# Optimization experiments

Hardware: AMD Instinct MI355X
Metric: run time of the kernel (lower is better)

The kernel has to match this reference:

```python
import jax, jax.numpy as jnp
import numpy as np

NINP, NHID, NPROJ, NLAYER = 240, 1024, 512, 3


def setup_inputs() -> dict:
    key = jax.random.key(0)
    keys = jax.random.split(key, 1 + NLAYER * 6)
    inp = {"x": jax.random.normal(keys[0], (500, 32, NINP), dtype=jnp.float32)}
    kit = iter(keys[1:])
    for l in range(NLAYER):
        nin = NINP if l == 0 else NPROJ
        s = 1.0 / np.sqrt(nin + NPROJ)
        inp[f"W{l}"] = jax.random.uniform(next(kit), (4 * NHID, nin + NPROJ), minval=-s, maxval=s, dtype=jnp.float32)
        inp[f"b{l}"] = jax.random.uniform(next(kit), (4 * NHID,), minval=-s, maxval=s, dtype=jnp.float32)
        sp = 1.0 / np.sqrt(NHID)
        inp[f"P{l}"] = jax.random.uniform(next(kit), (NPROJ, NHID), minval=-sp, maxval=sp, dtype=jnp.float32)
        inp[f"pi{l}"] = jax.random.normal(next(kit), (NHID,), dtype=jnp.float32) * 0.1
        inp[f"pf{l}"] = jax.random.normal(next(kit), (NHID,), dtype=jnp.float32) * 0.1
        inp[f"po{l}"] = jax.random.normal(next(kit), (NHID,), dtype=jnp.float32) * 0.1
    return inp


def _lstmp_layer(x, W, b, P, pi, pf, po):
    # x: [T, B, nin]; returns [T, B, nproj]
    T, B, _ = x.shape
    h0 = jnp.zeros((B, NPROJ), x.dtype)
    c0 = jnp.zeros((B, NHID), x.dtype)

    def step(carry, xt):
        hx, cx = carry
        gates = jnp.concatenate([xt, hx], axis=1) @ W.T + b  # [B, 4*nhid]
        c_in, i_g, f_g, o_g = jnp.split(gates, 4, axis=1)
        i_g = jax.nn.sigmoid(i_g + pi * cx)
        f_g = jax.nn.sigmoid(f_g + pf * cx)
        cy = jnp.clip(f_g * cx + i_g * jnp.tanh(c_in), -50.0, 50.0)
        o_g = jax.nn.sigmoid(o_g + po * cy)
        hy = (o_g * jnp.tanh(cy)) @ P.T  # [B, nproj]
        return (hy, cy), hy

    _, ys = jax.lax.scan(step, (h0, c0), x)
    return ys


def reference(x, W0, b0, P0, pi0, pf0, po0, W1, b1, P1, pi1, pf1, po1, W2, b2, P2, pi2, pf2, po2):
    y = _lstmp_layer(x, W0, b0, P0, pi0, pf0, po0)
    y = _lstmp_layer(y, W1, b1, P1, pi1, pf1, po1)
    y = _lstmp_layer(y, W2, b2, P2, pi2, pf2, po2)
    return y
```

## Files before the change

kernel.cpp:

```cpp
#include <hip/hip_runtime.h>


typedef short s16x4 __attribute__((ext_vector_type(4)));
typedef short s16x8 __attribute__((ext_vector_type(8)));
typedef float f32x4 __attribute__((ext_vector_type(4)));

#define MFMA16(a,b,c) __builtin_amdgcn_mfma_f32_16x16x32_bf16((a),(b),(c),0,0,0)

__device__ __forceinline__ unsigned short f2bf(float f) {
  unsigned int u = __builtin_bit_cast(unsigned int, f);
  u += 0x7FFFu + ((u >> 16) & 1u);
  return (unsigned short)(u >> 16);
}
__device__ __forceinline__ float bf2f(unsigned short h) {
  unsigned int u = ((unsigned int)h) << 16;
  return __builtin_bit_cast(float, u);
}
__device__ __forceinline__ float fsig(float x)  { return __fdividef(1.0f, 1.0f + __expf(-x)); }
__device__ __forceinline__ float ftanh(float x) { return 1.0f - __fdividef(2.0f, 1.0f + __expf(2.0f * x)); }

__device__ __forceinline__ void bload16(s16x8* dst, const unsigned short* p) {
  asm volatile("global_load_dwordx4 %0, %1, off sc1"
               : "=v"(*dst) : "v"(p) : "memory");
}
__device__ __forceinline__ void bwait() {
  asm volatile("s_waitcnt vmcnt(0)" ::: "memory");
  __builtin_amdgcn_sched_barrier(0);
}
__device__ __forceinline__ void bstore16(unsigned short* p, s16x8 v) {
  asm volatile("global_store_dwordx4 %0, %1, off sc1"
               :: "v"(p), "v"(v) : "memory");
}

__device__ __forceinline__ unsigned int cnt_load(const unsigned int* p) {
  return __hip_atomic_load(p, __ATOMIC_RELAXED, __HIP_MEMORY_SCOPE_AGENT);
}
__device__ __forceinline__ void cnt_add(unsigned int* p) {
  __hip_atomic_fetch_add(p, 1u, __ATOMIC_RELAXED, __HIP_MEMORY_SCOPE_AGENT);
}

__device__ __forceinline__ void gbar(unsigned int* bar, unsigned int* rel, unsigned int seq) {
  __syncthreads();
  asm volatile("" ::: "memory");
  if (blockIdx.x == 0) {
    const int tid = threadIdx.x;
    if (tid > 0 && tid < 192) {
      while (__hip_atomic_load(&bar[tid * 16], __ATOMIC_RELAXED, __HIP_MEMORY_SCOPE_AGENT) != seq) {
        __builtin_amdgcn_s_sleep(1);
      }
    }
    __syncthreads();
    if (tid == 0) {
      __hip_atomic_store(rel, seq, __ATOMIC_RELAXED, __HIP_MEMORY_SCOPE_AGENT);
    }
  } else {
    if (threadIdx.x == 0) {
      __hip_atomic_store(&bar[blockIdx.x * 16], seq, __ATOMIC_RELAXED, __HIP_MEMORY_SCOPE_AGENT);
      while (__hip_atomic_load(rel, __ATOMIC_RELAXED, __HIP_MEMORY_SCOPE_AGENT) != seq) {
        __builtin_amdgcn_s_sleep(1);
      }
    }
    __syncthreads();
  }
  asm volatile("" ::: "memory");
}

__global__ __launch_bounds__(512, 2) void lstmp_persist(
    const float* __restrict__ x,
    const float* __restrict__ W0, const float* __restrict__ b0, const float* __restrict__ P0,
    const float* __restrict__ pi0, const float* __restrict__ pf0, const float* __restrict__ po0,
    const float* __restrict__ W1, const float* __restrict__ b1, const float* __restrict__ P1,
    const float* __restrict__ pi1, const float* __restrict__ pf1, const float* __restrict__ po1,
    const float* __restrict__ W2, const float* __restrict__ b2, const float* __restrict__ P2,
    const float* __restrict__ pi2, const float* __restrict__ pf2, const float* __restrict__ po2,
    float* __restrict__ out, unsigned char* __restrict__ ws)
{
  const int tid  = threadIdx.x;
  const int bid  = blockIdx.x;
  const int lane = tid & 63;
  const int wv   = tid >> 6;
  const int quad8 = (lane >> 4) * 8;
  const int nrow  = lane & 15;

  unsigned int* bar   = (unsigned int*)ws;
  unsigned int* rel   = bar + 4096;
  unsigned int* gcnt  = rel + 32;
  unsigned int* mcnt  = gcnt + 128;
  unsigned short* xhi = (unsigned short*)(ws + 20480);
  unsigned short* xlo  = xhi  + 4096000;
  unsigned short* hhi  = xlo  + 4096000;
  unsigned short* hlo  = hhi  + 98304;
  unsigned short* mhi  = hlo  + 98304;
  unsigned short* mlo  = mhi  + 98304;

  const float* Wsrc[3] = {W0, W1, W2};
  const float* Psrc[3] = {P0, P1, P2};
  const float* Bsrc[3] = {b0, b1, b2};
  const float* PIs[3]  = {pi0, pi1, pi2};
  const float* PFs[3]  = {pf0, pf1, pf2};
  const float* POs[3]  = {po0, po1, po2};

  __shared__ float exch[8][4][512];
  __shared__ float c_lds[512];
  __shared__ float lds_pad[4096];
  ((volatile float*)lds_pad)[tid & 4095] = 0.0f;
  unsigned short* mst = (unsigned short*)lds_pad;
  unsigned short* hst = mst + 1024;

  const unsigned int NT = 192u * 512u;
  const unsigned int gtid = (unsigned int)bid * 512u + (unsigned int)tid;

  const int lA  = bid >> 6;
  const int utA = bid & 63;
  const int ptC = (bid & 63) >> 1;
  const int mtC = bid & 1;

  const int nkbinA  = (lA == 0) ? 8   : 16;
  const int kinpadA = (lA == 0) ? 256 : 512;
  const int kbwA    = (lA == 0) ? 3   : 4;
  const int kwA     = (lA == 0) ? 752 : 1024;
  const int ninA    = (lA == 0) ? 240 : 512;
  const int kb0     = wv * kbwA;

  for (unsigned int i = gtid; i < 4096000u; i += NT) {
    unsigned int k = i & 255u, tb = i >> 8;
    float v = (k < 240u) ? x[tb * 240u + k] : 0.0f;
    unsigned short h = f2bf(v);
    xhi[i] = h; xlo[i] = f2bf(v - bf2f(h));
  }
  for (unsigned int i = gtid; i < 98304u; i += NT) { hhi[i] = 0; hlo[i] = 0; }
  for (unsigned int i = gtid; i < 640u; i += NT) gcnt[i] = 0u;
  c_lds[tid] = 0.0f;

  s16x8 wgh[4][4], wgl[4][4];
  {
    const float* Wl = Wsrc[lA];
    #pragma unroll
    for (int j = 0; j < 4; ++j) {
      if (j < kbwA) {
        const int kbase = (kb0 + j) * 32 + quad8;
        #pragma unroll
        for (int g = 0; g < 4; ++g) {
          const size_t r = (size_t)((g * 64 + utA) * 16 + nrow);
          #pragma unroll
          for (int jj = 0; jj < 8; ++jj) {
            const int k = kbase + jj;
            float v;
            if (k < kinpadA) v = (lA == 0 && k >= 240) ? 0.0f : Wl[r * kwA + k];
            else             v = Wl[r * kwA + (k - kinpadA + ninA)];
            unsigned short h = f2bf(v);
            wgh[j][g][jj] = (short)h;
            wgl[j][g][jj] = (short)f2bf(v - bf2f(h));
          }
        }
      } else {
        #pragma unroll
        for (int g = 0; g < 4; ++g) { wgh[j][g] = (s16x8)0; wgl[j][g] = (s16x8)0; }
      }
    }
  }
  s16x8 wph[4], wpl[4];
  {
    const float* Pl = Psrc[lA];
    const size_t prow = (size_t)(ptC * 16 + nrow);
    #pragma unroll
    for (int j = 0; j < 4; ++j) {
      const int kbase = (wv * 4 + j) * 32 + quad8;
      #pragma unroll
      for (int jj = 0; jj < 8; ++jj) {
        float v = Pl[prow * 1024u + (size_t)(kbase + jj)];
        unsigned short h = f2bf(v);
        wph[j][jj] = (short)h;
        wpl[j][jj] = (short)f2bf(v - bf2f(h));
      }
    }
  }
  const int uc = utA * 16 + (tid & 15);
  const float rbc = Bsrc[lA][uc];
  const float rbi = Bsrc[lA][1024 + uc];
  const float rbf = Bsrc[lA][2048 + uc];
  const float rbo = Bsrc[lA][3072 + uc];
  const float rpi = PIs[lA][uc];
  const float rpf = PFs[lA][uc];
  const float rpo = POs[lA][uc];

  __builtin_amdgcn_fence(__ATOMIC_RELEASE, "agent");
  gbar(bar, rel, 1u);
  __builtin_amdgcn_fence(__ATOMIC_ACQUIRE, "agent");

  for (int s = 0; s < 502; ++s) {
    const int t = s - lA;
    const bool act = (t >= 0) && (t < 500);
    const int rbuf = (s + 1) & 1;
    const int wbuf = s & 1;

    if (act) {
      const unsigned short* hbh = hhi + rbuf * 49152;
      const unsigned short* hbl = hlo + rbuf * 49152;

      s16x8 fh0[4], fl0[4], fh1[4], fl1[4];
      #pragma unroll
      for (int j = 0; j < 4; ++j) {
        if (j < kbwA) {
          const int kb = kb0 + j;
          if (kb < nkbinA) {
            if (lA == 0) {
              const unsigned short* ph = xhi + (size_t)(t * 32 + nrow) * 256 + kb * 32 + quad8;
              const unsigned short* pl = xlo + (size_t)(t * 32 + nrow) * 256 + kb * 32 + quad8;
              fh0[j] = *(const s16x8*)ph; fh1[j] = *(const s16x8*)(ph + 16 * 256);
              fl0[j] = *(const s16x8*)pl; fl1[j] = *(const s16x8*)(pl + 16 * 256);
            } else {
              const unsigned short* ph = hbh + (size_t)((lA - 1) * 32 + nrow) * 512 + kb * 32 + quad8;
              const unsigned short* pl = hbl + (size_t)((lA - 1) * 32 + nrow) * 512 + kb * 32 + quad8;
              bload16(&fh0[j], ph); bload16(&fh1[j], ph + 16 * 512);
              bload16(&fl0[j], pl); bload16(&fl1[j], pl + 16 * 512);
            }
          } else {
            const int ko = kb * 32 + quad8 - kinpadA;
            const unsigned short* ph = hbh + (size_t)(lA * 32 + nrow) * 512 + ko;
            const unsigned short* pl = hbl + (size_t)(lA * 32 + nrow) * 512 + ko;
            bload16(&fh0[j], ph); bload16(&fh1[j], ph + 16 * 512);
            bload16(&fl0[j], pl); bload16(&fl1[j], pl + 16 * 512);
          }
        }
      }
      bwait();

      f32x4 acc[4][2];
      #pragma unroll
      for (int g = 0; g < 4; ++g) { acc[g][0] = {0.f,0.f,0.f,0.f}; acc[g][1] = {0.f,0.f,0.f,0.f}; }

      #pragma unroll
      for (int j = 0; j < 4; ++j) {
        if (j < kbwA) {
          #pragma unroll
          for (int g = 0; g < 4; ++g) {
            acc[g][0] = MFMA16(fh0[j], wgh[j][g], acc[g][0]);
            acc[g][0] = MFMA16(fl0[j], wgh[j][g], acc[g][0]);
            acc[g][0] = MFMA16(fh0[j], wgl[j][g], acc[g][0]);
            acc[g][1] = MFMA16(fh1[j], wgh[j][g], acc[g][1]);
            acc[g][1] = MFMA16(fl1[j], wgh[j][g], acc[g][1]);
            acc[g][1] = MFMA16(fh1[j], wgl[j][g], acc[g][1]);
          }
        }
      }
      #pragma unroll
      for (int g = 0; g < 4; ++g) {
        #pragma unroll
        for (int r = 0; r < 4; ++r) {
          const int m0 = (lane >> 4) * 4 + r;
          exch[wv][g][m0 * 16 + (lane & 15)]        = acc[g][0][r];
          exch[wv][g][(m0 + 16) * 16 + (lane & 15)] = acc[g][1][r];
        }
      }
      __syncthreads();

      {
        const int e = tid;
        float sc = 0.f, si = 0.f, sf = 0.f, so = 0.f;
        #pragma unroll
        for (int w = 0; w < 8; ++w) {
          sc += exch[w][0][e]; si += exch[w][1][e];
          sf += exch[w][2][e]; so += exch[w][3][e];
        }
        const float cin = sc + rbc;
        const float gi  = si + rbi;
        const float gf  = sf + rbf;
        const float go  = so + rbo;
        const float cx  = c_lds[e];
        const float ig  = fsig(gi + rpi * cx);
        const float fg  = fsig(gf + rpf * cx);
        float cy = fg * cx + ig * ftanh(cin);
        cy = fminf(50.0f, fmaxf(-50.0f, cy));
        const float og = fsig(go + rpo * cy);
        const float mv = og * ftanh(cy);
        c_lds[e] = cy;
        const unsigned short mh = f2bf(mv);
        mst[e]       = mh;
        mst[512 + e] = f2bf(mv - bf2f(mh));
      }
      __syncthreads();
      if (tid < 128) {
        const int plane = tid >> 6;
        const int r2 = tid & 63;
        const int bl = r2 >> 1, half = r2 & 1;
        s16x8 v = *(const s16x8*)(mst + plane * 512 + bl * 16 + half * 8);
        unsigned short* dst = (plane ? mlo : mhi) + (size_t)(lA * 32 + bl) * 1024 + utA * 16 + half * 8;
        bstore16(dst, v);
        asm volatile("s_waitcnt vmcnt(0)" ::: "memory");
      }
      __syncthreads();
      if (tid == 0) cnt_add(&mcnt[lA * 128 + (utA & 3) * 32]);

      if (tid == 0) {
        const unsigned int want = 64u * (unsigned int)(t + 1);
        const unsigned int* mp = mcnt + lA * 128;
        for (;;) {
          unsigned int sum = cnt_load(mp) + cnt_load(mp + 32) + cnt_load(mp + 64) + cnt_load(mp + 96);
          if (sum >= want) break;
          __builtin_amdgcn_s_sleep(1);
        }
      }
      __syncthreads();

      const unsigned short* mah = mhi + (size_t)(lA * 32 + mtC * 16 + nrow) * 1024;
      const unsigned short* mal = mlo + (size_t)(lA * 32 + mtC * 16 + nrow) * 1024;

      s16x8 fmh[4], fml[4];
      #pragma unroll
      for (int j = 0; j < 4; ++j) {
        const int ko = (wv * 4 + j) * 32 + quad8;
        bload16(&fmh[j], mah + ko);
        bload16(&fml[j], mal + ko);
      }
      bwait();

      f32x4 pacc = {0.f, 0.f, 0.f, 0.f};
      #pragma unroll
      for (int j = 0; j < 4; ++j) {
        pacc = MFMA16(fmh[j], wph[j], pacc);
        pacc = MFMA16(fml[j], wph[j], pacc);
        pacc = MFMA16(fmh[j], wpl[j], pacc);
      }
      #pragma unroll
      for (int r = 0; r < 4; ++r) {
        exch[wv][0][((lane >> 4) * 4 + r) * 16 + (lane & 15)] = pacc[r];
      }
      __syncthreads();
      if (tid < 256) {
        float v = 0.f;
        #pragma unroll
        for (int w = 0; w < 8; ++w) v += exch[w][0][tid];
        const unsigned short hh = f2bf(v);
        hst[tid]       = hh;
        hst[256 + tid] = f2bf(v - bf2f(hh));
        if (lA == 2) {
          const int b = mtC * 16 + (tid >> 4);
          const int p = ptC * 16 + (tid & 15);
          out[((size_t)t * 32 + b) * 512 + p] = v;
        }
      }
      __syncthreads();
      if (tid < 64) {
        const int plane = tid >> 5;
        const int r2 = tid & 31;
        const int bl = r2 >> 1, half = r2 & 1;
        s16x8 v = *(const s16x8*)(hst + plane * 256 + bl * 16 + half * 8);
        unsigned short* dst = (plane ? hlo : hhi) + (size_t)wbuf * 49152
                            + (size_t)(lA * 32 + mtC * 16 + bl) * 512 + ptC * 16 + half * 8;
        bstore16(dst, v);
        asm volatile("s_waitcnt vmcnt(0)" ::: "memory");
      }
    }
    __syncthreads();
    if (tid == 0) {
      cnt_add(&gcnt[(bid & 3) * 32]);
      const unsigned int want = 192u * (unsigned int)(s + 1);
      for (;;) {
        unsigned int sum = cnt_load(gcnt) + cnt_load(gcnt + 32) + cnt_load(gcnt + 64) + cnt_load(gcnt + 96);
        if (sum >= want) break;
        __builtin_amdgcn_s_sleep(1);
      }
    }
    __syncthreads();
  }
}

extern "C" void kernel_launch(void* const* d_in, const int* in_sizes, int n_in,
                              void* d_out, int out_size, void* d_ws, size_t ws_size,
                              hipStream_t stream) {
  const float* x   = (const float*)d_in[0];
  const float* W0  = (const float*)d_in[1];
  const float* b0  = (const float*)d_in[2];
  const float* P0  = (const float*)d_in[3];
  const float* pi0 = (const float*)d_in[4];
  const float* pf0 = (const float*)d_in[5];
  const float* po0 = (const float*)d_in[6];
  const float* W1  = (const float*)d_in[7];
  const float* b1  = (const float*)d_in[8];
  const float* P1  = (const float*)d_in[9];
  const float* pi1 = (const float*)d_in[10];
  const float* pf1 = (const float*)d_in[11];
  const float* po1 = (const float*)d_in[12];
  const float* W2  = (const float*)d_in[13];
  const float* b2  = (const float*)d_in[14];
  const float* P2  = (const float*)d_in[15];
  const float* pi2 = (const float*)d_in[16];
  const float* pf2 = (const float*)d_in[17];
  const float* po2 = (const float*)d_in[18];

  hipLaunchKernelGGL(lstmp_persist, dim3(192), dim3(512), 0, stream,
                     x, W0, b0, P0, pi0, pf0, po0,
                     W1, b1, P1, pi1, pf1, po1,
                     W2, b2, P2, pi2, pf2, po2,
                     (float*)d_out, (unsigned char*)d_ws);
}
```

Before: 8.106 ms.

## Replace global per-step barrier with per-layer counters and 4-deep h buffers

Removes the grid-wide barrier that every block joined at each wavefront step. Each layer group now waits only on its own layer's previous step, the upstream layer's current output, and the downstream layer's progress (back-pressure). Hidden state buffers grow from 2 to 4 slots so layers can drift apart by several timesteps without overwriting data still being read. This decouples the three layers' pipelines and lowers synchronization stalls, at the cost of more workspace and more complex ordering logic.

After: 8.025 ms. Within noise of the previous version (-1.0%).

```diff
diff --git a/kernel.cpp b/kernel.cpp
--- a/kernel.cpp
+++ b/kernel.cpp
@@ -37,6 +37,13 @@
 }
 __device__ __forceinline__ void cnt_add(unsigned int* p) {
   __hip_atomic_fetch_add(p, 1u, __ATOMIC_RELAXED, __HIP_MEMORY_SCOPE_AGENT);
+}
+__device__ __forceinline__ void poll4(const unsigned int* p, unsigned int want) {
+  for (;;) {
+    unsigned int s = cnt_load(p) + cnt_load(p + 32) + cnt_load(p + 64) + cnt_load(p + 96);
+    if (s >= want) break;
+    __builtin_amdgcn_s_sleep(1);
+  }
 }
 
 __device__ __forceinline__ void gbar(unsigned int* bar, unsigned int* rel, unsigned int seq) {
@@ -84,13 +91,13 @@
 
   unsigned int* bar   = (unsigned int*)ws;
   unsigned int* rel   = bar + 4096;
-  unsigned int* gcnt  = rel + 32;
-  unsigned int* mcnt  = gcnt + 128;
+  unsigned int* lcnt  = rel + 32;
+  unsigned int* mcnt  = lcnt + 384;
   unsigned short* xhi = (unsigned short*)(ws + 20480);
   unsigned short* xlo  = xhi  + 4096000;
   unsigned short* hhi  = xlo  + 4096000;
-  unsigned short* hlo  = hhi  + 98304;
-  unsigned short* mhi  = hlo  + 98304;
+  unsigned short* hlo  = hhi  + 196608;
+  unsigned short* mhi  = hlo  + 196608;
   unsigned short* mlo  = mhi  + 98304;
 
   const float* Wsrc[3] = {W0, W1, W2};
@@ -128,8 +135,8 @@
     unsigned short h = f2bf(v);
     xhi[i] = h; xlo[i] = f2bf(v - bf2f(h));
   }
-  for (unsigned int i = gtid; i < 98304u; i += NT) { hhi[i] = 0; hlo[i] = 0; }
-  for (unsigned int i = gtid; i < 640u; i += NT) gcnt[i] = 0u;
+  for (unsigned int i = gtid; i < 196608u; i += NT) { hhi[i] = 0; hlo[i] = 0; }
+  for (unsigned int i = gtid; i < 768u; i += NT) lcnt[i] = 0u;
   c_lds[tid] = 0.0f;
 
   s16x8 wgh[4][4], wgl[4][4];
@@ -188,181 +195,173 @@
   gbar(bar, rel, 1u);
   __builtin_amdgcn_fence(__ATOMIC_ACQUIRE, "agent");
 
-  for (int s = 0; s < 502; ++s) {
-    const int t = s - lA;
-    const bool act = (t >= 0) && (t < 500);
-    const int rbuf = (s + 1) & 1;
-    const int wbuf = s & 1;
-
-    if (act) {
-      const unsigned short* hbh = hhi + rbuf * 49152;
-      const unsigned short* hbl = hlo + rbuf * 49152;
-
-      s16x8 fh0[4], fl0[4], fh1[4], fl1[4];
-      #pragma unroll
-      for (int j = 0; j < 4; ++j) {
-        if (j < kbwA) {
-          const int kb = kb0 + j;
-          if (kb < nkbinA) {
-            if (lA == 0) {
-              const unsigned short* ph = xhi + (size_t)(t * 32 + nrow) * 256 + kb * 32 + quad8;
-              const unsigned short* pl = xlo + (size_t)(t * 32 + nrow) * 256 + kb * 32 + quad8;
-              fh0[j] = *(const s16x8*)ph; fh1[j] = *(const s16x8*)(ph + 16 * 256);
-              fl0[j] = *(const s16x8*)pl; fl1[j] = *(const s16x8*)(pl + 16 * 256);
-            } else {
-              const unsigned short* ph = hbh + (size_t)((lA - 1) * 32 + nrow) * 512 + kb * 32 + quad8;
-              const unsigned short* pl = hbl + (size_t)((lA - 1) * 32 + nrow) * 512 + kb * 32 + quad8;
-              bload16(&fh0[j], ph); bload16(&fh1[j], ph + 16 * 512);
-              bload16(&fl0[j], pl); bload16(&fl1[j], pl + 16 * 512);
-            }
+  for (int t = 0; t < 500; ++t) {
+    if (tid == 0) {
+      poll4(lcnt + lA * 128, 64u * (unsigned int)t);
+      if (lA > 0) poll4(lcnt + (lA - 1) * 128, 64u * (unsigned int)(t + 1));
+      if (lA < 2 && t >= 4) poll4(lcnt + (lA + 1) * 128, 64u * (unsigned int)(t - 3));
+    }
+    __syncthreads();
+
+    const unsigned short* hRecH = hhi + (size_t)(((t + 3) & 3) * 49152 + lA * 16384);
+    const unsigned short* hRecL = hlo + (size_t)(((t + 3) & 3) * 49152 + lA * 16384);
+    const unsigned short* hInH  = hhi + (size_t)((t & 3) * 49152 + (lA - 1) * 16384);
+    const unsigned short* hInL  = hlo + (size_t)((t & 3) * 49152 + (lA - 1) * 16384);
+
+    s16x8 fh0[4], fl0[4], fh1[4], fl1[4];
+    #pragma unroll
+    for (int j = 0; j < 4; ++j) {
+      if (j < kbwA) {
+        const int kb = kb0 + j;
+        if (kb < nkbinA) {
+          if (lA == 0) {
+            const unsigned short* ph = xhi + (size_t)(t * 32 + nrow) * 256 + kb * 32 + quad8;
+            const unsigned short* pl = xlo + (size_t)(t * 32 + nrow) * 256 + kb * 32 + quad8;
+            fh0[j] = *(const s16x8*)ph; fh1[j] = *(const s16x8*)(ph + 16 * 256);
+            fl0[j] = *(const s16x8*)pl; fl1[j] = *(const s16x8*)(pl + 16 * 256);
           } else {
-            const int ko = kb * 32 + quad8 - kinpadA;
-            const unsigned short* ph = hbh + (size_t)(lA * 32 + nrow) * 512 + ko;
-            const unsigned short* pl = hbl + (size_t)(lA * 32 + nrow) * 512 + ko;
+            const unsigned short* ph = hInH + (size_t)nrow * 512 + kb * 32 + quad8;
+            const unsigned short* pl = hInL + (size_t)nrow * 512 + kb * 32 + quad8;
             bload16(&fh0[j], ph); bload16(&fh1[j], ph + 16 * 512);
             bload16(&fl0[j], pl); bload16(&fl1[j], pl + 16 * 512);
           }
+        } else {
+          const int ko = kb * 32 + quad8 - kinpadA;
+          const unsigned short* ph = hRecH + (size_t)nrow * 512 + ko;
+          const unsigned short* pl = hRecL + (size_t)nrow * 512 + ko;
+          bload16(&fh0[j], ph); bload16(&fh1[j], ph + 16 * 512);
+          bload16(&fl0[j], pl); bload16(&fl1[j], pl + 16 * 512);
         }
       }
-      bwait();
-
-      f32x4 acc[4][2];
-      #pragma unroll
-      for (int g = 0; g < 4; ++g) { acc[g][0] = {0.f,0.f,0.f,0.f}; acc[g][1] = {0.f,0.f,0.f,0.f}; }
-
-      #pragma unroll
-      for (int j = 0; j < 4; ++j) {
-        if (j < kbwA) {
-          #pragma unroll
-          for (int g = 0; g < 4; ++g) {
-            acc[g][0] = MFMA16(fh0[j], wgh[j][g], acc[g][0]);
-            acc[g][0] = MFMA16(fl0[j], wgh[j][g], acc[g][0]);
-            acc[g][0] = MFMA16(fh0[j], wgl[j][g], acc[g][0]);
-            acc[g][1] = MFMA16(fh1[j], wgh[j][g], acc[g][1]);
-            acc[g][1] = MFMA16(fl1[j], wgh[j][g], acc[g][1]);
-            acc[g][1] = MFMA16(fh1[j], wgl[j][g], acc[g][1]);
-          }
+    }
+    bwait();
+
+    f32x4 acc[4][2];
+    #pragma unroll
+    for (int g = 0; g < 4; ++g) { acc[g][0] = {0.f,0.f,0.f,0.f}; acc[g][1] = {0.f,0.f,0.f,0.f}; }
+
+    #pragma unroll
+    for (int j = 0; j < 4; ++j) {
+      if (j < kbwA) {
+        #pragma unroll
+        for (int g = 0; g < 4; ++g) {
+          acc[g][0] = MFMA16(fh0[j], wgh[j][g], acc[g][0]);
+          acc[g][0] = MFMA16(fl0[j], wgh[j][g], acc[g][0]);
+          acc[g][0] = MFMA16(fh0[j], wgl[j][g], acc[g][0]);
+          acc[g][1] = MFMA16(fh1[j], wgh[j][g], acc[g][1]);
+          acc[g][1] = MFMA16(fl1[j], wgh[j][g], acc[g][1]);
+          acc[g][1] = MFMA16(fh1[j], wgl[j][g], acc[g][1]);
         }
       }
-      #pragma unroll
-      for (int g = 0; g < 4; ++g) {
-        #pragma unroll
-        for (int r = 0; r < 4; ++r) {
-          const int m0 = (lane >> 4) * 4 + r;
-          exch[wv][g][m0 * 16 + (lane & 15)]        = acc[g][0][r];
-          exch[wv][g][(m0 + 16) * 16 + (lane & 15)] = acc[g][1][r];
-        }
-      }
-      __syncthreads();
-
-      {
-        const int e = tid;
-        float sc = 0.f, si = 0.f, sf = 0.f, so = 0.f;
-        #pragma unroll
-        for (int w = 0; w < 8; ++w) {
-          sc += exch[w][0][e]; si += exch[w][1][e];
-          sf += exch[w][2][e]; so += exch[w][3][e];
-        }
-        const float cin = sc + rbc;
-        const float gi  = si + rbi;
-        const float gf  = sf + rbf;
-        const float go  = so + rbo;
-        const float cx  = c_lds[e];
-        const float ig  = fsig(gi + rpi * cx);
-        const float fg  = fsig(gf + rpf * cx);
-        float cy = fg * cx + ig * ftanh(cin);
-        cy = fminf(50.0f, fmaxf(-50.0f, cy));
-        const float og = fsig(go + rpo * cy);
-        const float mv = og * ftanh(cy);
-        c_lds[e] = cy;
-        const unsigned short mh = f2bf(mv);
-        mst[e]       = mh;
-        mst[512 + e] = f2bf(mv - bf2f(mh));
-      }
-      __syncthreads();
-      if (tid < 128) {
-        const int plane = tid >> 6;
-        const int r2 = tid & 63;
-        const int bl = r2 >> 1, half = r2 & 1;
-        s16x8 v = *(const s16x8*)(mst + plane * 512 + bl * 16 + half * 8);
-        unsigned short* dst = (plane ? mlo : mhi) + (size_t)(lA * 32 + bl) * 1024 + utA * 16 + half * 8;
-        bstore16(dst, v);
-        asm volatile("s_waitcnt vmcnt(0)" ::: "memory");
-      }
-      __syncthreads();
-      if (tid == 0) cnt_add(&mcnt[lA * 128 + (utA & 3) * 32]);
-
-      if (tid == 0) {
-        const unsigned int want = 64u * (unsigned int)(t + 1);
-        const unsigned int* mp = mcnt + lA * 128;
-        for (;;) {
-          unsigned int sum = cnt_load(mp) + cnt_load(mp + 32) + cnt_load(mp + 64) + cnt_load(mp + 96);
-          if (sum >= want) break;
-          __builtin_amdgcn_s_sleep(1);
-        }
-      }
-      __syncthreads();
-
-      const unsigned short* mah = mhi + (size_t)(lA * 32 + mtC * 16 + nrow) * 1024;
-      const unsigned short* mal = mlo + (size_t)(lA * 32 + mtC * 16 + nrow) * 1024;
-
-      s16x8 fmh[4], fml[4];
-      #pragma unroll
-      for (int j = 0; j < 4; ++j) {
-        const int ko = (wv * 4 + j) * 32 + quad8;
-        bload16(&fmh[j], mah + ko);
-        bload16(&fml[j], mal + ko);
-      }
-      bwait();
-
-      f32x4 pacc = {0.f, 0.f, 0.f, 0.f};
-      #pragma unroll
-      for (int j = 0; j < 4; ++j) {
-        pacc = MFMA16(fmh[j], wph[j], pacc);
-        pacc = MFMA16(fml[j], wph[j], pacc);
-        pacc = MFMA16(fmh[j], wpl[j], pacc);
-      }
+    }
+    #pragma unroll
+    for (int g = 0; g < 4; ++g) {
       #pragma unroll
       for (int r = 0; r < 4; ++r) {
-        exch[wv][0][((lane >> 4) * 4 + r) * 16 + (lane & 15)] = pacc[r];
-      }
-      __syncthreads();
-      if (tid < 256) {
-        float v = 0.f;
-        #pragma unroll
-        for (int w = 0; w < 8; ++w) v += exch[w][0][tid];
-        const unsigned short hh = f2bf(v);
-        hst[tid]       = hh;
-        hst[256 + tid] = f2bf(v - bf2f(hh));
-        if (lA == 2) {
-          const int b = mtC * 16 + (tid >> 4);
-          const int p = ptC * 16 + (tid & 15);
-          out[((size_t)t * 32 + b) * 512 + p] = v;
-        }
-      }
-      __syncthreads();
-      if (tid < 64) {
-        const int plane = tid >> 5;
-        const int r2 = tid & 31;
-        const int bl = r2 >> 1, half = r2 & 1;
-        s16x8 v = *(const s16x8*)(hst + plane * 256 + bl * 16 + half * 8);
-        unsigned short* dst = (plane ? hlo : hhi) + (size_t)wbuf * 49152
-                            + (size_t)(lA * 32 + mtC * 16 + bl) * 512 + ptC * 16 + half * 8;
-        bstore16(dst, v);
-        asm volatile("s_waitcnt vmcnt(0)" ::: "memory");
-      }
+        const int m0 = (lane >> 4) * 4 + r;
+        exch[wv][g][m0 * 16 + (lane & 15)]        = acc[g][0][r];
+        exch[wv][g][(m0 + 16) * 16 + (lane & 15)] = acc[g][1][r];
+      }
+    }
+    __syncthreads();
+
+    {
+      const int e = tid;
+      float sc = 0.f, si = 0.f, sf = 0.f, so = 0.f;
+      #pragma unroll
+      for (int w = 0; w < 8; ++w) {
+        sc += exch[w][0][e]; si += exch[w][1][e];
+        sf += exch[w][2][e]; so += exch[w][3][e];
+      }
+      const float cin = sc + rbc;
+      const float gi  = si + rbi;
+      const float gf  = sf + rbf;
+      const float go  = so + rbo;
+      const float cx  = c_lds[e];
+      const float ig  = fsig(gi + rpi * cx);
+      const float fg  = fsig(gf + rpf * cx);
+      float cy = fg * cx + ig * ftanh(cin);
+      cy = fminf(50.0f, fmaxf(-50.0f, cy));
+      const float og = fsig(go + rpo * cy);
+      const float mv = og * ftanh(cy);
+      c_lds[e] = cy;
+      const unsigned short mh = f2bf(mv);
+      mst[e]       = mh;
+      mst[512 + e] = f2bf(mv - bf2f(mh));
+    }
+    __syncthreads();
+    if (tid < 128) {
+      const int plane = tid >> 6;
+      const int r2 = tid & 63;
+      const int bl = r2 >> 1, half = r2 & 1;
+      s16x8 v = *(const s16x8*)(mst + plane * 512 + bl * 16 + half * 8);
+      unsigned short* dst = (plane ? mlo : mhi) + (size_t)(lA * 32 + bl) * 1024 + utA * 16 + half * 8;
+      bstore16(dst, v);
+      asm volatile("s_waitcnt vmcnt(0)" ::: "memory");
     }
     __syncthreads();
     if (tid == 0) {
-      cnt_add(&gcnt[(bid & 3) * 32]);
-      const unsigned int want = 192u * (unsigned int)(s + 1);
-      for (;;) {
-        unsigned int sum = cnt_load(gcnt) + cnt_load(gcnt + 32) + cnt_load(gcnt + 64) + cnt_load(gcnt + 96);
-        if (sum >= want) break;
-        __builtin_amdgcn_s_sleep(1);
-      }
-    }
-    __syncthreads();
+      cnt_add(&mcnt[lA * 128 + (utA & 3) * 32]);
+      poll4(mcnt + lA * 128, 64u * (unsigned int)(t + 1));
+    }
+    __syncthreads();
+
+    const unsigned short* mah = mhi + (size_t)(lA * 32 + mtC * 16 + nrow) * 1024;
+    const unsigned short* mal = mlo + (size_t)(lA * 32 + mtC * 16 + nrow) * 1024;
+
+    s16x8 fmh[4], fml[4];
+    #pragma unroll
+    for (int j = 0; j < 4; ++j) {
+      const int ko = (wv * 4 + j) * 32 + quad8;
+      bload16(&fmh[j], mah + ko);
+      bload16(&fml[j], mal + ko);
+    }
+    bwait();
+
+    f32x4 pacc = {0.f, 0.f, 0.f, 0.f};
+    #pragma unroll
+    for (int j = 0; j < 4; ++j) {
+      pacc = MFMA16(fmh[j], wph[j], pacc);
+      pacc = MFMA16(fml[j], wph[j], pacc);
+      pacc = MFMA16(fmh[j], wpl[j], pacc);
+    }
+    #pragma unroll
+    for (int r = 0; r < 4; ++r) {
+      exch[wv][0][((lane >> 4) * 4 + r) * 16 + (lane & 15)] = pacc[r];
+    }
+    __syncthreads();
+    if (tid < 256) {
+      float v = 0.f;
+      #pragma unroll
+      for (int w = 0; w < 8; ++w) v += exch[w][0][tid];
+      const unsigned short hh = f2bf(v);
+      hst[tid]       = hh;
+      hst[256 + tid] = f2bf(v - bf2f(hh));
+      if (lA == 2) {
+        const int b = mtC * 16 + (tid >> 4);
+        const int p = ptC * 16 + (tid & 15);
+        out[((size_t)t * 32 + b) * 512 + p] = v;
+      }
+    }
+    __syncthreads();
+    if (tid < 64) {
+      const int plane = tid >> 5;
+      const int r2 = tid & 31;
+      const int bl = r2 >> 1, half = r2 & 1;
+      s16x8 v = *(const s16x8*)(hst + plane * 256 + bl * 16 + half * 8);
+      unsigned short* dst = (plane ? hlo : hhi) + (size_t)((t & 3) * 49152 + lA * 16384)
+                          + (size_t)(mtC * 16 + bl) * 512 + ptC * 16 + half * 8;
+      bstore16(dst, v);
+      asm volatile("s_waitcnt vmcnt(0)" ::: "memory");
+    }
+    __syncthreads();
+    if (tid == 0) cnt_add(&lcnt[lA * 128 + (utA & 3) * 32]);
+  }
+
+  __syncthreads();
+  if (tid == 0) {
+    __hip_atomic_store(&bar[bid * 16], 0u, __ATOMIC_RELAXED, __HIP_MEMORY_SCOPE_AGENT);
+    if (bid == 0) __hip_atomic_store(rel, 0u, __ATOMIC_RELAXED, __HIP_MEMORY_SCOPE_AGENT);
   }
 }
 
```
